# Kernel optimization log

Hardware: AMD Instinct MI355X
Metric: run time of the kernel (lower is better)

The kernel has to match this reference:

```python
import jax, jax.numpy as jnp
import numpy as np

N = 50000
IN_DIM = 128
HID = 64
HEADS = 4
OUT_DIM = 2
NEG_SLOPE = 0.2


def setup_inputs() -> dict:
    key = jax.random.key(0)
    ks = jax.random.split(key, 10)
    x = jax.random.normal(ks[0], (N, IN_DIM), dtype=jnp.float32)
    edge_index = jax.random.randint(ks[1], (2, 800000), 0, N, dtype=jnp.int64)
    s = 0.1
    W1 = jax.random.normal(ks[2], (IN_DIM, HEADS * HID), dtype=jnp.float32) * s
    att_src1 = jax.random.normal(ks[3], (HEADS, HID), dtype=jnp.float32) * s
    att_dst1 = jax.random.normal(ks[4], (HEADS, HID), dtype=jnp.float32) * s
    b1 = jnp.zeros((HEADS * HID,), dtype=jnp.float32)
    W2 = jax.random.normal(ks[5], (HEADS * HID, 1 * OUT_DIM), dtype=jnp.float32) * s
    att_src2 = jax.random.normal(ks[6], (1, OUT_DIM), dtype=jnp.float32) * s
    att_dst2 = jax.random.normal(ks[7], (1, OUT_DIM), dtype=jnp.float32) * s
    b2 = jnp.zeros((OUT_DIM,), dtype=jnp.float32)
    return {"x": x, "edge_index": edge_index, "W1": W1, "att_src1": att_src1,
            "att_dst1": att_dst1, "b1": b1, "W2": W2, "att_src2": att_src2,
            "att_dst2": att_dst2, "b2": b2}


def gat_conv(x, W, att_src, att_dst, b, src, dst, heads, ch):
    # x: [N, F_in] -> h: [N, H, C]
    n = x.shape[0]
    h = (x @ W).reshape(n, heads, ch)
    a_s = jnp.einsum('nhc,hc->nh', h, att_src)  # [N, H]
    a_d = jnp.einsum('nhc,hc->nh', h, att_dst)  # [N, H]
    e = jax.nn.leaky_relu(a_s[src] + a_d[dst], NEG_SLOPE)  # [E, H]
    # segment softmax over incoming edges of each destination node
    m = jax.ops.segment_max(e, dst, num_segments=n)
    ex = jnp.exp(e - m[dst])
    z = jax.ops.segment_sum(ex, dst, num_segments=n)
    alpha = ex / z[dst]  # [E, H]
    msg = h[src] * alpha[:, :, None]  # [E, H, C]
    out = jax.ops.segment_sum(msg, dst, num_segments=n)  # [N, H, C]
    return out.reshape(n, heads * ch) + b


def reference(x, edge_index, W1, att_src1, att_dst1, b1, W2, att_src2, att_dst2, b2):
    n = x.shape[0]
    loop = jnp.arange(n, dtype=edge_index.dtype)
    src = jnp.concatenate([edge_index[0], loop])  # add_self_loops (PyG default)
    dst = jnp.concatenate([edge_index[1], loop])
    h = gat_conv(x, W1, att_src1, att_dst1, b1, src, dst, HEADS, HID)
    h = jax.nn.elu(h)
    # dropout is identity at inference
    out = gat_conv(h, W2, att_src2, att_dst2, b2, src, dst, 1, OUT_DIM)
    return out
```

## Files before the change

kernel.cpp:

```cpp
#include <hip/hip_runtime.h>

#define NN     50000
#define E_RAW  800000
#define ETOT   (E_RAW + NN)
#define FIN    128
#define FH     256
#define NEG    0.2f
#define BCAP   64

#define P_PART 8
#define DPW    6250
#define R_REP  32
#define EPW    (E_RAW / R_REP)
#define CNT_WGS (P_PART * R_REP)
#define PREP_WGS 8
#define OFF_NB  ((NN + 255) / 256)
#define GEMM_NB ((NN + 63) / 64)

typedef __attribute__((ext_vector_type(8))) short s16x8;
typedef __attribute__((ext_vector_type(4))) float f32x4;

static __device__ __forceinline__ float leaky(float v) { return v > 0.f ? v : NEG * v; }

static __device__ __forceinline__ unsigned short f2bf(float f) {
    unsigned u = __float_as_uint(f);
    unsigned r = u + 0x7fffu + ((u >> 16) & 1u);
    return (unsigned short)(r >> 16);
}

__global__ __launch_bounds__(1024) void k_count(const int* __restrict__ ei,
                                                const float* __restrict__ W1,
                                                unsigned short* __restrict__ Wt_bf,
                                                int* __restrict__ pcnt)
{
    const int t = threadIdx.x;
    if (blockIdx.x >= CNT_WGS) {
        const int base = (blockIdx.x - CNT_WGS) * 4096;
        for (int i = t; i < 4096; i += 1024) {
            int idx = base + i;
            int k = idx >> 8, col = idx & 255;
            Wt_bf[col * FIN + k] = f2bf(W1[k * FH + col]);
        }
        return;
    }
    __shared__ int lcnt[DPW];
    const int p  = blockIdx.x >> 5;
    const int r  = blockIdx.x & 31;
    const int lo = p * DPW;
    for (int i = t; i < DPW; i += 1024) lcnt[i] = 0;
    __syncthreads();
    const int ebase = r * EPW, eend = ebase + EPW;
    for (int e0 = ebase + t * 4; e0 < eend; e0 += 4096) {
        int4 dv4 = *(const int4*)&ei[E_RAW + e0];
#pragma unroll
        for (int k = 0; k < 4; k++) {
            unsigned rel = (unsigned)((&dv4.x)[k] - lo);
            if (rel < DPW) atomicAdd(&lcnt[rel], 1);
        }
    }
    __syncthreads();
    for (int i = t; i < DPW; i += 1024)
        pcnt[r * NN + lo + i] = lcnt[i];
}

__global__ __launch_bounds__(256) void k_gx(const float* __restrict__ x,
                                            const unsigned short* __restrict__ Wt_bf,
                                            const float* __restrict__ att_src,
                                            const float* __restrict__ att_dst,
                                            const int* __restrict__ pcnt,
                                            int* __restrict__ soff,
                                            int* __restrict__ cnt,
                                            int* __restrict__ csr_src,
                                            unsigned short* __restrict__ h1b,
                                            float* __restrict__ a_s,
                                            float* __restrict__ a_d)
{
    const int t = threadIdx.x;
    if (blockIdx.x < OFF_NB) {
        int d = blockIdx.x * 256 + t;
        if (d >= NN) return;
        int run = 1;
#pragma unroll
        for (int r = 0; r < R_REP; r++) {
            soff[r * NN + d] = run;
            run += pcnt[r * NN + d];
        }
        cnt[d] = run;
        csr_src[(size_t)d << 6] = d;
        return;
    }

    __shared__ unsigned short Sbuf[64 * 256];
    const int w    = t >> 6;
    const int lane = t & 63;
    const int li   = lane & 15;
    const int q8   = (lane >> 4) * 8;
    const int quad = lane >> 4;
    const int n0   = (blockIdx.x - OFF_NB) * 64;

    {
        const int node_l = t >> 2;
        const int k0 = (t & 3) * 32;
        int nn = n0 + node_l; if (nn >= NN) nn = NN - 1;
        const float* xp = &x[(size_t)nn * FIN + k0];
        unsigned short* xd = &Sbuf[node_l * 136 + k0];
#pragma unroll
        for (int i = 0; i < 8; i++) {
            float4 v = *(const float4*)&xp[i * 4];
            xd[i * 4 + 0] = f2bf(v.x);
            xd[i * 4 + 1] = f2bf(v.y);
            xd[i * 4 + 2] = f2bf(v.z);
            xd[i * 4 + 3] = f2bf(v.w);
        }
    }
    __syncthreads();

    f32x4 acc[4][4];
#pragma unroll
    for (int i = 0; i < 4; i++)
#pragma unroll
        for (int j = 0; j < 4; j++) acc[i][j] = (f32x4){0.f, 0.f, 0.f, 0.f};

#pragma unroll
    for (int kki = 0; kki < 4; kki++) {
        const int kk = kki * 32;
        s16x8 af[4], bf[4];
#pragma unroll
        for (int n16 = 0; n16 < 4; n16++) {
            int col = w * 64 + n16 * 16 + li;
            bf[n16] = *(const s16x8*)&Wt_bf[col * FIN + kk + q8];
        }
#pragma unroll
        for (int m16 = 0; m16 < 4; m16++)
            af[m16] = *(const s16x8*)&Sbuf[(m16 * 16 + li) * 136 + kk + q8];
#pragma unroll
        for (int m16 = 0; m16 < 4; m16++)
#pragma unroll
            for (int n16 = 0; n16 < 4; n16++)
                acc[m16][n16] = __builtin_amdgcn_mfma_f32_16x16x32_bf16(
                    af[m16], bf[n16], acc[m16][n16], 0, 0, 0);
    }

    {
        float as_c[4], ad_c[4];
#pragma unroll
        for (int n16 = 0; n16 < 4; n16++) {
            int col = w * 64 + n16 * 16 + li;
            as_c[n16] = att_src[col];
            ad_c[n16] = att_dst[col];
        }
#pragma unroll
        for (int m16 = 0; m16 < 4; m16++) {
            float ps[4], pd[4];
#pragma unroll
            for (int reg = 0; reg < 4; reg++) {
                float s = 0.f, d = 0.f;
#pragma unroll
                for (int n16 = 0; n16 < 4; n16++) {
                    s += acc[m16][n16][reg] * as_c[n16];
                    d += acc[m16][n16][reg] * ad_c[n16];
                }
                ps[reg] = s; pd[reg] = d;
            }
#pragma unroll
            for (int off = 1; off < 16; off <<= 1) {
#pragma unroll
                for (int reg = 0; reg < 4; reg++) {
                    ps[reg] += __shfl_xor(ps[reg], off);
                    pd[reg] += __shfl_xor(pd[reg], off);
                }
            }
            if (li == 0) {
#pragma unroll
                for (int reg = 0; reg < 4; reg++) {
                    int node = n0 + m16 * 16 + quad * 4 + reg;
                    if (node < NN) {
                        a_s[node * 4 + w] = ps[reg];
                        a_d[node * 4 + w] = pd[reg];
                    }
                }
            }
        }
    }

    __syncthreads();
#pragma unroll
    for (int m16 = 0; m16 < 4; m16++)
#pragma unroll
        for (int n16 = 0; n16 < 4; n16++)
#pragma unroll
            for (int reg = 0; reg < 4; reg++)
                Sbuf[(m16 * 16 + quad * 4 + reg) * FH + w * 64 + n16 * 16 + li] =
                    f2bf(acc[m16][n16][reg]);
    __syncthreads();
    {
        const int node_l = t >> 2;
        const int c0 = (t & 3) * 64;
        int node = n0 + node_l;
        if (node < NN) {
#pragma unroll
            for (int i = 0; i < 8; i++)
                *(uint4*)&h1b[(size_t)node * FH + c0 + i * 8] =
                    *(const uint4*)&Sbuf[node_l * FH + c0 + i * 8];
        }
    }
}

__global__ __launch_bounds__(1024) void k_scat2(const int* __restrict__ ei,
                                                const int* __restrict__ soff,
                                                int* __restrict__ csr_src)
{
    __shared__ int cur[DPW];
    const int t  = threadIdx.x;
    const int p  = blockIdx.x >> 5;
    const int r  = blockIdx.x & 31;
    const int lo = p * DPW;
    for (int i = t; i < DPW; i += 1024)
        cur[i] = soff[r * NN + lo + i];
    __syncthreads();
    const int ebase = r * EPW, eend = ebase + EPW;
    for (int e0 = ebase + t * 4; e0 < eend; e0 += 4096) {
        int4 sv4 = *(const int4*)&ei[e0];
        int4 dv4 = *(const int4*)&ei[E_RAW + e0];
#pragma unroll
        for (int k = 0; k < 4; k++) {
            int d = (&dv4.x)[k];
            unsigned rel = (unsigned)(d - lo);
            if (rel < DPW) {
                int pos = atomicAdd(&cur[rel], 1);
                if (pos < BCAP)
                    csr_src[((size_t)d << 6) + pos] = (&sv4.x)[k];
            }
        }
    }
}

__global__ __launch_bounds__(256) void k_agg1(const int* __restrict__ cnt,
                                              const int* __restrict__ csr_src,
                                              const float* __restrict__ a_s1,
                                              const float* __restrict__ a_d1,
                                              const unsigned short* __restrict__ h1b,
                                              const float* __restrict__ b1,
                                              const float* __restrict__ W2,
                                              const float* __restrict__ att_src2,
                                              const float* __restrict__ att_dst2,
                                              float4* __restrict__ nd4)
{
    const int lane = threadIdx.x & 63;
    const int n = blockIdx.x * 4 + (threadIdx.x >> 6);
    if (n >= NN) return;
    int m = cnt[n]; if (m > BCAP) m = BCAP;
    const int h = lane >> 4;
    const float ad_h = a_d1[n * 4 + h];
    float acc0 = 0.f, acc1 = 0.f, acc2 = 0.f, acc3 = 0.f, z = 0.f;
    const int* sp = &csr_src[(size_t)n << 6];
#pragma unroll 4
    for (int j = 0; j < m; j++) {
        int s = sp[j];
        float as_h = a_s1[s * 4 + h];
        float ex = __expf(leaky(as_h + ad_h));
        unsigned long long wv =
            *(const unsigned long long*)(h1b + (size_t)s * FH + lane * 4);
        unsigned lo = (unsigned)wv, hi = (unsigned)(wv >> 32);
        acc0 += __uint_as_float(lo << 16) * ex;
        acc1 += __uint_as_float(lo & 0xffff0000u) * ex;
        acc2 += __uint_as_float(hi << 16) * ex;
        acc3 += __uint_as_float(hi & 0xffff0000u) * ex;
        z += ex;
    }
    const int c0 = lane * 4;
    float4 bb = *(const float4*)&b1[c0];
    float v0 = acc0 / z + bb.x;
    float v1 = acc1 / z + bb.y;
    float v2 = acc2 / z + bb.z;
    float v3 = acc3 / z + bb.w;
    v0 = v0 > 0.f ? v0 : __expf(v0) - 1.f;
    v1 = v1 > 0.f ? v1 : __expf(v1) - 1.f;
    v2 = v2 > 0.f ? v2 : __expf(v2) - 1.f;
    v3 = v3 > 0.f ? v3 : __expf(v3) - 1.f;
    float4 w2a = *(const float4*)&W2[c0 * 2];
    float4 w2b = *(const float4*)&W2[c0 * 2 + 4];
    float s0 = v0 * w2a.x + v1 * w2a.z + v2 * w2b.x + v3 * w2b.z;
    float s1 = v0 * w2a.y + v1 * w2a.w + v2 * w2b.y + v3 * w2b.w;
#pragma unroll
    for (int off = 32; off; off >>= 1) {
        s0 += __shfl_xor(s0, off);
        s1 += __shfl_xor(s1, off);
    }
    if (lane == 0) {
        float4 nd;
        nd.x = s0; nd.y = s1;
        nd.z = s0 * att_src2[0] + s1 * att_src2[1];
        nd.w = s0 * att_dst2[0] + s1 * att_dst2[1];
        nd4[n] = nd;
    }
}

__global__ __launch_bounds__(256) void k_agg2(const int* __restrict__ cnt,
                                              const int* __restrict__ csr_src,
                                              const float4* __restrict__ nd4,
                                              const float* __restrict__ b2,
                                              float* __restrict__ out)
{
    const int l = threadIdx.x & 15;
    const int n = blockIdx.x * 16 + (threadIdx.x >> 4);
    if (n >= NN) return;
    int m = cnt[n]; if (m > BCAP) m = BCAP;
    const int* sp = &csr_src[(size_t)n << 6];
    const float ad = nd4[n].w;
    float z = 0.f, a0 = 0.f, a1 = 0.f;
    for (int j = l; j < m; j += 16) {
        int s = sp[j];
        float4 f = nd4[s];
        float ex = __expf(leaky(f.z + ad));
        z  += ex;
        a0 += f.x * ex;
        a1 += f.y * ex;
    }
#pragma unroll
    for (int off = 8; off; off >>= 1) {
        z  += __shfl_xor(z, off);
        a0 += __shfl_xor(a0, off);
        a1 += __shfl_xor(a1, off);
    }
    if (l == 0) {
        out[n * 2 + 0] = a0 / z + b2[0];
        out[n * 2 + 1] = a1 / z + b2[1];
    }
}

extern "C" void kernel_launch(void* const* d_in, const int* in_sizes, int n_in,
                              void* d_out, int out_size, void* d_ws, size_t ws_size,
                              hipStream_t stream)
{
    const float* x        = (const float*)d_in[0];
    const int*   ei       = (const int*)d_in[1];
    const float* W1       = (const float*)d_in[2];
    const float* att_src1 = (const float*)d_in[3];
    const float* att_dst1 = (const float*)d_in[4];
    const float* b1       = (const float*)d_in[5];
    const float* W2       = (const float*)d_in[6];
    const float* att_src2 = (const float*)d_in[7];
    const float* att_dst2 = (const float*)d_in[8];
    const float* b2       = (const float*)d_in[9];
    float* out = (float*)d_out;

    int*    csr_src = (int*)d_ws;
    unsigned short* h1b = (unsigned short*)(csr_src + (size_t)NN * 64);
    unsigned short* Wt_bf = h1b + (size_t)NN * FH;
    int*    pcnt  = (int*)(Wt_bf + FH * FIN);
    int*    soff  = pcnt + (size_t)NN * R_REP;
    int*    cnt   = soff + (size_t)NN * R_REP;
    float*  a_s1  = (float*)(cnt + NN);
    float*  a_d1  = a_s1 + (size_t)NN * 4;
    float4* nd4   = (float4*)(a_d1 + (size_t)NN * 4);

    k_count<<<CNT_WGS + PREP_WGS, 1024, 0, stream>>>(ei, W1, Wt_bf, pcnt);
    k_gx<<<OFF_NB + GEMM_NB, 256, 0, stream>>>(x, Wt_bf, att_src1, att_dst1,
                                               pcnt, soff, cnt, csr_src,
                                               h1b, a_s1, a_d1);
    k_scat2<<<CNT_WGS, 1024, 0, stream>>>(ei, soff, csr_src);
    k_agg1<<<(NN + 3) / 4, 256, 0, stream>>>(cnt, csr_src, a_s1, a_d1, h1b,
                                             b1, W2, att_src2, att_dst2, nd4);
    k_agg2<<<(NN + 15) / 16, 256, 0, stream>>>(cnt, csr_src, nd4, b2, out);
}
```

Before: 205.3 us.

## Remap layer-1 aggregation to 16 lanes per node with wide bf16 loads

Each destination node in k_agg1 is now handled by 16 lanes instead of a full 64-lane wavefront, so one wave covers four nodes. Each lane loads 32 bytes of bf16 features and keeps 16 accumulators. Neighbor indices are loaded cooperatively, 16 at a time, and broadcast with shuffles; the next batch is prefetched. The reduction shrinks to 16 lanes. The goal is fewer wavefronts, wider memory transactions and less per-edge index traffic, at the cost of more registers and wasted lanes when nodes in a wave have different degrees.

New measurement: 212.7 us. 3.6% more time.

```diff
diff --git a/kernel.cpp b/kernel.cpp
--- a/kernel.cpp
+++ b/kernel.cpp
@@ -246,48 +246,89 @@
                                               const float* __restrict__ att_dst2,
                                               float4* __restrict__ nd4)
 {
-    const int lane = threadIdx.x & 63;
-    const int n = blockIdx.x * 4 + (threadIdx.x >> 6);
-    if (n >= NN) return;
+    const int t    = threadIdx.x;
+    const int lane = t & 63;
+    const int sl   = lane & 15;
+    const int n    = blockIdx.x * 16 + (t >> 4);
     int m = cnt[n]; if (m > BCAP) m = BCAP;
-    const int h = lane >> 4;
+    const int h  = sl >> 2;
+    const int c0 = sl << 4;
     const float ad_h = a_d1[n * 4 + h];
-    float acc0 = 0.f, acc1 = 0.f, acc2 = 0.f, acc3 = 0.f, z = 0.f;
     const int* sp = &csr_src[(size_t)n << 6];
-#pragma unroll 4
-    for (int j = 0; j < m; j++) {
-        int s = sp[j];
-        float as_h = a_s1[s * 4 + h];
-        float ex = __expf(leaky(as_h + ad_h));
-        unsigned long long wv =
-            *(const unsigned long long*)(h1b + (size_t)s * FH + lane * 4);
-        unsigned lo = (unsigned)wv, hi = (unsigned)(wv >> 32);
-        acc0 += __uint_as_float(lo << 16) * ex;
-        acc1 += __uint_as_float(lo & 0xffff0000u) * ex;
-        acc2 += __uint_as_float(hi << 16) * ex;
-        acc3 += __uint_as_float(hi & 0xffff0000u) * ex;
-        z += ex;
-    }
-    const int c0 = lane * 4;
-    float4 bb = *(const float4*)&b1[c0];
-    float v0 = acc0 / z + bb.x;
-    float v1 = acc1 / z + bb.y;
-    float v2 = acc2 / z + bb.z;
-    float v3 = acc3 / z + bb.w;
-    v0 = v0 > 0.f ? v0 : __expf(v0) - 1.f;
-    v1 = v1 > 0.f ? v1 : __expf(v1) - 1.f;
-    v2 = v2 > 0.f ? v2 : __expf(v2) - 1.f;
-    v3 = v3 > 0.f ? v3 : __expf(v3) - 1.f;
-    float4 w2a = *(const float4*)&W2[c0 * 2];
-    float4 w2b = *(const float4*)&W2[c0 * 2 + 4];
-    float s0 = v0 * w2a.x + v1 * w2a.z + v2 * w2b.x + v3 * w2b.z;
-    float s1 = v0 * w2a.y + v1 * w2a.w + v2 * w2b.y + v3 * w2b.w;
-#pragma unroll
-    for (int off = 32; off; off >>= 1) {
+
+    int mmax = m;
+    mmax = max(mmax, __shfl_xor(mmax, 16));
+    mmax = max(mmax, __shfl_xor(mmax, 32));
+
+    float acc[16];
+#pragma unroll
+    for (int i = 0; i < 16; i++) acc[i] = 0.f;
+    float z = 0.f;
+
+    int sv = sp[sl];
+    for (int jb = 0; jb < mmax; jb += 16) {
+        int svn = 0;
+        if (jb + 16 < mmax) svn = sp[sl + jb + 16];
+        int lim = mmax - jb; if (lim > 16) lim = 16;
+        for (int j4 = 0; j4 < lim; j4 += 4) {
+#pragma unroll
+            for (int u = 0; u < 4; u++) {
+                const int jj = j4 + u;
+                const int j  = jb + jj;
+                int s = __shfl(sv, (lane & 48) + jj);
+                const bool live = j < m;
+                s = live ? s : 0;
+                float ex = __expf(leaky(a_s1[s * 4 + h] + ad_h));
+                ex = live ? ex : 0.f;
+                const unsigned short* hp = h1b + ((size_t)s << 8) + c0;
+                uint4 r0 = *(const uint4*)hp;
+                uint4 r1 = *(const uint4*)(hp + 8);
+                acc[0]  += __uint_as_float(r0.x << 16)         * ex;
+                acc[1]  += __uint_as_float(r0.x & 0xffff0000u) * ex;
+                acc[2]  += __uint_as_float(r0.y << 16)         * ex;
+                acc[3]  += __uint_as_float(r0.y & 0xffff0000u) * ex;
+                acc[4]  += __uint_as_float(r0.z << 16)         * ex;
+                acc[5]  += __uint_as_float(r0.z & 0xffff0000u) * ex;
+                acc[6]  += __uint_as_float(r0.w << 16)         * ex;
+                acc[7]  += __uint_as_float(r0.w & 0xffff0000u) * ex;
+                acc[8]  += __uint_as_float(r1.x << 16)         * ex;
+                acc[9]  += __uint_as_float(r1.x & 0xffff0000u) * ex;
+                acc[10] += __uint_as_float(r1.y << 16)         * ex;
+                acc[11] += __uint_as_float(r1.y & 0xffff0000u) * ex;
+                acc[12] += __uint_as_float(r1.z << 16)         * ex;
+                acc[13] += __uint_as_float(r1.z & 0xffff0000u) * ex;
+                acc[14] += __uint_as_float(r1.w << 16)         * ex;
+                acc[15] += __uint_as_float(r1.w & 0xffff0000u) * ex;
+                z += ex;
+            }
+        }
+        sv = svn;
+    }
+
+    const float rz = 1.0f / z;
+    float s0 = 0.f, s1 = 0.f;
+#pragma unroll
+    for (int i = 0; i < 16; i += 4) {
+        float4 bb = *(const float4*)&b1[c0 + i];
+        float v0 = acc[i]     * rz + bb.x;
+        float v1 = acc[i + 1] * rz + bb.y;
+        float v2 = acc[i + 2] * rz + bb.z;
+        float v3 = acc[i + 3] * rz + bb.w;
+        v0 = v0 > 0.f ? v0 : __expf(v0) - 1.f;
+        v1 = v1 > 0.f ? v1 : __expf(v1) - 1.f;
+        v2 = v2 > 0.f ? v2 : __expf(v2) - 1.f;
+        v3 = v3 > 0.f ? v3 : __expf(v3) - 1.f;
+        float4 wa = *(const float4*)&W2[(c0 + i) * 2];
+        float4 wb = *(const float4*)&W2[(c0 + i) * 2 + 4];
+        s0 += v0 * wa.x + v1 * wa.z + v2 * wb.x + v3 * wb.z;
+        s1 += v0 * wa.y + v1 * wa.w + v2 * wb.y + v3 * wb.w;
+    }
+#pragma unroll
+    for (int off = 1; off < 16; off <<= 1) {
         s0 += __shfl_xor(s0, off);
         s1 += __shfl_xor(s1, off);
     }
-    if (lane == 0) {
+    if (sl == 0) {
         float4 nd;
         nd.x = s0; nd.y = s1;
         nd.z = s0 * att_src2[0] + s1 * att_src2[1];
@@ -360,7 +401,7 @@
                                                pcnt, soff, cnt, csr_src,
                                                h1b, a_s1, a_d1);
     k_scat2<<<CNT_WGS, 1024, 0, stream>>>(ei, soff, csr_src);
-    k_agg1<<<(NN + 3) / 4, 256, 0, stream>>>(cnt, csr_src, a_s1, a_d1, h1b,
-                                             b1, W2, att_src2, att_dst2, nd4);
+    k_agg1<<<NN / 16, 256, 0, stream>>>(cnt, csr_src, a_s1, a_d1, h1b,
+                                        b1, W2, att_src2, att_dst2, nd4);
     k_agg2<<<(NN + 15) / 16, 256, 0, stream>>>(cnt, csr_src, nd4, b2, out);
 }
```
